# Optimization experiments

Hardware: AMD Instinct MI355X
Metric: run time of the kernel (lower is better)

The kernel has to match this reference:

```python
import jax, jax.numpy as jnp
import numpy as np
import math

H, W = 64, 64
WS = 8            # window_size
KS = 8            # kernel_size (depthwise conv stride=kernel)
D = 512           # d_model
CF = 128          # flow_dModel
IC = D + CF       # 640
HEAD = 8
GH, GW = H // WS, W // WS
G = GH * GW       # windows
EPS = 1e-5


def layernorm(x, g, b):
    m = jnp.mean(x, axis=-1, keepdims=True)
    v = jnp.mean((x - m) ** 2, axis=-1, keepdims=True)
    return (x - m) * jax.lax.rsqrt(v + EPS) * g + b


def depthwise_conv(x_nchw, w, b):
    # w: [C, 1, KS, KS], stride=KS, VALID, groups=C
    y = jax.lax.conv_general_dilated(
        x_nchw, w, window_strides=(KS, KS), padding='VALID',
        feature_group_count=x_nchw.shape[1],
        dimension_numbers=('NCHW', 'OIHW', 'NCHW'))
    return y + b[None, :, None, None]


def setup_inputs() -> dict:
    key = jax.random.key(0)
    ks = jax.random.split(key, 24)
    bt = 8
    s = 0.02
    inp = {
        'x': jax.random.normal(ks[0], (bt, H * W, D), jnp.float32),
        'f': jax.random.normal(ks[1], (bt, H * W, CF), jnp.float32),
        't': 2,
        'Wq': jax.random.normal(ks[2], (IC, D), jnp.float32) * s,
        'bq': jnp.zeros((D,), jnp.float32),
        'Wk': jax.random.normal(ks[3], (IC, D), jnp.float32) * s,
        'bk': jnp.zeros((D,), jnp.float32),
        'Wv': jax.random.normal(ks[4], (D, D), jnp.float32) * s,
        'bv': jnp.zeros((D,), jnp.float32),
        'Wo': jax.random.normal(ks[5], (D, D), jnp.float32) * s,
        'bo': jnp.zeros((D,), jnp.float32),
        'convK_w': jax.random.normal(ks[6], (IC, 1, KS, KS), jnp.float32) * s,
        'convK_b': jnp.zeros((IC,), jnp.float32),
        'convV_w': jax.random.normal(ks[7], (D, 1, KS, KS), jnp.float32) * s,
        'convV_b': jnp.zeros((D,), jnp.float32),
        'qn_g': jnp.ones((IC,), jnp.float32), 'qn_b': jnp.zeros((IC,), jnp.float32),
        'kn_g': jnp.ones((IC,), jnp.float32), 'kn_b': jnp.zeros((IC,), jnp.float32),
        'vn_g': jnp.ones((D,), jnp.float32), 'vn_b': jnp.zeros((D,), jnp.float32),
        'rw_W': jax.random.normal(ks[8], (IC, CF), jnp.float32) * s,
        'rw_b': jnp.zeros((CF,), jnp.float32),
    }
    return inp


def reference(x, f, t, Wq, bq, Wk, bk, Wv, bv, Wo, bo,
              convK_w, convK_b, convV_w, convV_b,
              qn_g, qn_b, kn_g, kn_b, vn_g, vn_b, rw_W, rw_b):
    bt, n, c = x.shape
    hd = c // HEAD
    x4 = x.reshape(bt, H, W, c)            # no padding: H, W multiples of WS
    f4 = f.reshape(bt, H, W, CF)

    xf = jnp.concatenate([x4, f4], axis=-1)                 # [bt,H,W,IC]
    flow_w = jax.nn.sigmoid(xf @ rw_W + rw_b)               # [bt,H,W,CF]
    f4 = f4 * flow_w
    qk = jnp.concatenate([x4, f4], axis=-1)                 # [bt,H,W,IC]

    def windows(a):
        cc = a.shape[-1]
        a = a.reshape(bt, GH, WS, GW, WS, cc).transpose(0, 1, 3, 2, 4, 5)
        return a.reshape(bt, G, WS * WS, cc)

    q = windows(qk)                                          # [bt,G,ws2,IC]

    k_glob = depthwise_conv(qk.transpose(0, 3, 1, 2), convK_w, convK_b)
    k_glob = k_glob.transpose(0, 2, 3, 1).reshape(bt, -1, IC)  # [bt,M,IC]
    M = k_glob.shape[1]
    k_glob = jnp.broadcast_to(k_glob[:, None], (bt, G, M, IC))
    k = jnp.concatenate([q, k_glob], axis=2)                 # [bt,G,ws2+M,IC]

    q = layernorm(q, qn_g, qn_b)
    k = layernorm(k, kn_g, kn_b)

    v_glob = depthwise_conv(x4.transpose(0, 3, 1, 2), convV_w, convV_b)
    v_glob = v_glob.transpose(0, 2, 3, 1).reshape(bt, -1, c)
    v_glob = jnp.broadcast_to(v_glob[:, None], (bt, G, M, c))
    xw = windows(x4)
    v = jnp.concatenate([xw, v_glob], axis=2)                # [bt,G,ws2+M,c]
    v = layernorm(v, vn_g, vn_b)

    query = q @ Wq + bq                                      # [bt,G,ws2,c]
    key = k @ Wk + bk
    value = v @ Wv + bv

    Lk = key.shape[2]
    query = query.reshape(bt, G, WS * WS, HEAD, hd).transpose(0, 1, 3, 2, 4)
    key = key.reshape(bt, G, Lk, HEAD, hd).transpose(0, 1, 3, 2, 4)
    value = value.reshape(bt, G, Lk, HEAD, hd).transpose(0, 1, 3, 2, 4)

    scores = jnp.einsum('bghqd,bghkd->bghqk', query, key) / math.sqrt(hd)
    attn = jax.nn.softmax(scores, axis=-1)
    out = jnp.einsum('bghqk,bghkd->bghqd', attn, value)      # [bt,G,H,ws2,hd]

    out = out.transpose(0, 1, 3, 2, 4).reshape(bt, GH, GW, WS, WS, c)
    out = out.transpose(0, 1, 3, 2, 4, 5).reshape(bt, H, W, c).reshape(bt, n, c)
    return out @ Wo + bo
```

## Files before the change

### kernel.cpp

```cpp
#include <hip/hip_runtime.h>
#include <hip/hip_bf16.h>

typedef __hip_bfloat16 bf16;
typedef __attribute__((ext_vector_type(8))) short bf16x8;
typedef __attribute__((ext_vector_type(8))) unsigned short ushort8;
typedef __attribute__((ext_vector_type(4))) float f32x4;

#define BT 8
#define HH 64
#define WW 64
#define NSP (HH*WW)
#define DD 512
#define CF 128
#define IC 640
#define NG 64
#define NM 64
#define EPS 1e-5f

static __device__ __forceinline__ float b2f(bf16 v) { return __bfloat162float(v); }
static __device__ __forceinline__ bf16 f2b(float v) { return __float2bfloat16(v); }
static __device__ __forceinline__ float u2f(unsigned short u) {
    return __uint_as_float((unsigned)u << 16);
}
static __device__ __forceinline__ unsigned short f2u(float v) {
    bf16 b = __float2bfloat16(v);
    return __builtin_bit_cast(unsigned short, b);
}

__global__ void detect_dtype(const void* __restrict__ x, int* __restrict__ flag) {
    __shared__ int cnt;
    if (threadIdx.x == 0) cnt = 0;
    __syncthreads();
    const unsigned* w = (const unsigned*)x;
    int local = 0;
    for (int i = threadIdx.x; i < 4096; i += 256) {
        float v = __uint_as_float(w[i]);
        float a = fabsf(v);
        if (a > 1e-5f && a < 1e4f) local++;
    }
    atomicAdd(&cnt, local);
    __syncthreads();
    if (threadIdx.x == 0) *flag = (cnt > 2048) ? 1 : 0;
}

#define NW 20
struct WTab {
    const void* src[NW];
    int pre[NW + 1];
};

__global__ void convert_weights(WTab t, const int* __restrict__ flag,
                                bf16* __restrict__ dst, int total) {
    int fp32 = *flag;
    for (int idx = blockIdx.x * blockDim.x + threadIdx.x; idx < total;
         idx += gridDim.x * blockDim.x) {
        int seg = 0;
        #pragma unroll
        for (int i = 0; i < NW; ++i) if (idx >= t.pre[i + 1]) seg = i + 1;
        int local = idx - t.pre[seg];
        bf16 v;
        if (fp32) v = f2b(((const float*)t.src[seg])[local]);
        else      v = ((const bf16*)t.src[seg])[local];
        dst[idx] = v;
    }
}

struct TT {
    int srcoff[5], dstoff[5], R[5], C[5], tpre[6];
};
__global__ void transpose_weights(const bf16* __restrict__ wc, bf16* __restrict__ wt, TT t) {
    __shared__ unsigned short tile[32][33];
    int tb = blockIdx.x;
    int seg = 0;
    while (tb >= t.tpre[seg + 1]) seg++;
    int lt = tb - t.tpre[seg];
    int R = t.R[seg], C = t.C[seg];
    int tpr = C / 32;
    int r0 = (lt / tpr) * 32, c0 = (lt % tpr) * 32;
    const unsigned short* src = (const unsigned short*)(wc + t.srcoff[seg]);
    unsigned short* dst = (unsigned short*)(wt + t.dstoff[seg]);
    int tx = threadIdx.x & 31, ty = threadIdx.x >> 5;
    #pragma unroll
    for (int i = 0; i < 4; ++i)
        tile[ty + i * 8][tx] = src[(long long)(r0 + ty + i * 8) * C + c0 + tx];
    __syncthreads();
    #pragma unroll
    for (int i = 0; i < 4; ++i)
        dst[(long long)(c0 + ty + i * 8) * R + r0 + tx] = tile[tx][ty + i * 8];
}

__global__ void fold_ln_weights(bf16* __restrict__ WT, const bf16* __restrict__ g,
                                const bf16* __restrict__ b, const bf16* __restrict__ bias,
                                float* __restrict__ colsum, float* __restrict__ bias2,
                                int K) {
    int n = blockIdx.x;
    bf16* wrow = WT + (long long)n * K;
    float s1 = 0.f, s2 = 0.f;
    for (int k = threadIdx.x; k < K; k += 256) {
        float w = b2f(wrow[k]);
        float gk = b2f(g[k]);
        wrow[k] = f2b(w * gk);
        s1 += w * gk;
        s2 += w * b2f(b[k]);
    }
    __shared__ float r1[256], r2[256];
    r1[threadIdx.x] = s1; r2[threadIdx.x] = s2;
    __syncthreads();
    for (int off = 128; off > 0; off >>= 1) {
        if (threadIdx.x < off) {
            r1[threadIdx.x] += r1[threadIdx.x + off];
            r2[threadIdx.x] += r2[threadIdx.x + off];
        }
        __syncthreads();
    }
    if (threadIdx.x == 0) {
        colsum[n] = r1[0];
        bias2[n]  = b2f(bias[n]) + r2[0];
    }
}

__global__ void assemble_qk_v(const void* __restrict__ xv, const void* __restrict__ fv,
                              const int* __restrict__ flag, bf16* __restrict__ qk,
                              int rows, long long xoff, long long foff) {
    int fp32 = *flag;
    long long total = (long long)rows * 80;
    for (long long i = (long long)blockIdx.x * blockDim.x + threadIdx.x; i < total;
         i += (long long)gridDim.x * blockDim.x) {
        int row = (int)(i / 80);
        int g = (int)(i % 80);
        ushort8 o;
        if (g < 64) {
            long long s = xoff + (long long)row * DD + g * 8;
            if (fp32) {
                const float* xp = (const float*)xv + s;
                #pragma unroll
                for (int e = 0; e < 8; ++e) o[e] = f2u(xp[e]);
            } else {
                o = *(const ushort8*)((const unsigned short*)xv + s);
            }
        } else {
            long long s = foff + (long long)row * CF + (g - 64) * 8;
            if (fp32) {
                const float* fp = (const float*)fv + s;
                #pragma unroll
                for (int e = 0; e < 8; ++e) o[e] = f2u(fp[e]);
            } else {
                o = *(const ushort8*)((const unsigned short*)fv + s);
            }
        }
        *(ushort8*)((unsigned short*)qk + (long long)row * IC + g * 8) = o;
    }
}

__global__ void reweight_v(bf16* __restrict__ qk, const bf16* __restrict__ fw, int rows) {
    long long total = (long long)rows * 16;
    long long i = (long long)blockIdx.x * blockDim.x + threadIdx.x;
    if (i >= total) return;
    int row = (int)(i / 16);
    int g = (int)(i % 16);
    unsigned short* qp = (unsigned short*)qk + (long long)row * IC + DD + g * 8;
    const unsigned short* wp = (const unsigned short*)fw + (long long)row * CF + g * 8;
    ushort8 qv = *(ushort8*)qp;
    ushort8 wv = *(const ushort8*)wp;
    #pragma unroll
    for (int e = 0; e < 8; ++e) qv[e] = f2u(u2f(qv[e]) * u2f(wv[e]));
    *(ushort8*)qp = qv;
}

__global__ void dwconv_kernel(const bf16* __restrict__ src, int ldr, int C, int ldout,
                              const bf16* __restrict__ w, const bf16* __restrict__ bias,
                              bf16* __restrict__ dst) {
    int bm = blockIdx.x;
    int b = bm >> 6;
    int m = bm & 63;
    int my = m >> 3, mx = m & 7;
    const bf16* sb = src + (long long)b * NSP * ldr;
    for (int c = threadIdx.x; c < C; c += blockDim.x) {
        float acc = b2f(bias[c]);
        #pragma unroll
        for (int ky = 0; ky < 8; ++ky) {
            #pragma unroll
            for (int kx = 0; kx < 8; ++kx) {
                int pos = (my * 8 + ky) * WW + mx * 8 + kx;
                acc += b2f(sb[(long long)pos * ldr + c]) * b2f(w[c * 64 + ky * 8 + kx]);
            }
        }
        dst[(long long)bm * ldout + c] = f2b(acc);
    }
}

__global__ void stats_fused(const bf16* __restrict__ qk, float* __restrict__ stats_full,
                            float* __restrict__ stats_x, int rows) {
    int gt = blockIdx.x * blockDim.x + threadIdx.x;
    int wid = gt >> 6;
    int lane = gt & 63;
    if (wid >= rows) return;
    const unsigned short* p = (const unsigned short*)qk + (long long)wid * IC;
    ushort8 v = *(const ushort8*)(p + lane * 8);
    float s1 = 0.f, ss1 = 0.f, s2 = 0.f, ss2 = 0.f;
    #pragma unroll
    for (int e = 0; e < 8; ++e) { float f = u2f(v[e]); s1 += f; ss1 += f * f; }
    if (lane < 16) {
        ushort8 v2 = *(const ushort8*)(p + DD + lane * 8);
        #pragma unroll
        for (int e = 0; e < 8; ++e) { float f = u2f(v2[e]); s2 += f; ss2 += f * f; }
    }
    #pragma unroll
    for (int off = 32; off > 0; off >>= 1) {
        s1  += __shfl_down(s1,  off, 64);
        ss1 += __shfl_down(ss1, off, 64);
        s2  += __shfl_down(s2,  off, 64);
        ss2 += __shfl_down(ss2, off, 64);
    }
    if (lane == 0) {
        float m1 = s1 / 512.f;
        float var1 = ss1 / 512.f - m1 * m1;
        stats_x[wid * 2]     = m1;
        stats_x[wid * 2 + 1] = rsqrtf(var1 + EPS);
        float st = s1 + s2, sst = ss1 + ss2;
        float m2 = st / 640.f;
        float var2 = sst / 640.f - m2 * m2;
        stats_full[wid * 2]     = m2;
        stats_full[wid * 2 + 1] = rsqrtf(var2 + EPS);
    }
}

__global__ void stats_kernel(const bf16* __restrict__ X, int lda, float* __restrict__ stats,
                             int rows, int K) {
    int gt = blockIdx.x * blockDim.x + threadIdx.x;
    int wid = gt >> 6;
    int lane = gt & 63;
    if (wid >= rows) return;
    const bf16* p = X + (long long)wid * lda;
    float s = 0.f, ss = 0.f;
    for (int k = lane; k < K; k += 64) {
        float v = b2f(p[k]);
        s += v; ss += v * v;
    }
    #pragma unroll
    for (int off = 32; off > 0; off >>= 1) {
        s  += __shfl_down(s,  off, 64);
        ss += __shfl_down(ss, off, 64);
    }
    if (lane == 0) {
        float m = s / K;
        float var = ss / K - m * m;
        stats[wid * 2]     = m;
        stats[wid * 2 + 1] = rsqrtf(var + EPS);
    }
}

__global__ __launch_bounds__(256)
void gemm_mfma(const bf16* __restrict__ A, int lda,
               const float* __restrict__ stats,
               const float* __restrict__ colsum,
               const float* __restrict__ bias2,
               const bf16* __restrict__ Bmat,
               const bf16* __restrict__ bias,
               bf16* __restrict__ C,
               void* __restrict__ Cout, const int* __restrict__ outflag, long long outoff,
               const bf16* __restrict__ A2, const float* __restrict__ stats2,
               bf16* __restrict__ C2, int M2,
               int M, int N, int K, int mode) {
    __shared__ unsigned short As[128 * 32];
    __shared__ unsigned short Bs[128 * 32];
    int tid = threadIdx.x;

    int nwgx = gridDim.x;
    int nwg = nwgx * gridDim.y;
    int orig = blockIdx.y * nwgx + blockIdx.x;
    int qq = nwg >> 3, rr = nwg & 7;
    int xcd = orig & 7, idx = orig >> 3;
    int wg = (xcd < rr ? xcd * (qq + 1) : rr * (qq + 1) + (xcd - rr) * qq) + idx;
    int gy = wg / nwgx;
    int gx = wg % nwgx;
    int bn = gx * 128;

    int nby_main = M >> 7;
    const bf16* Ap;
    const float* stp;
    int rowbase, mlim, glob;
    if (gy < nby_main) {
        Ap = A; stp = stats; rowbase = gy * 128; mlim = M; glob = 0;
    } else {
        Ap = A2; stp = stats2; rowbase = (gy - nby_main) * 128; mlim = M2; glob = 1;
    }

    int wave = tid >> 6, lane = tid & 63;
    int qm = (wave >> 1) * 64;
    int qn = (wave & 1) * 64;
    int lm = lane & 15;
    int kq = (lane >> 4) * 8;
    int sr = lane >> 2;
    int sc = (lane & 3) * 8;

    f32x4 acc[4][4];
    #pragma unroll
    for (int i = 0; i < 4; ++i)
        #pragma unroll
        for (int j = 0; j < 4; ++j)
            acc[i][j] = (f32x4){0.f, 0.f, 0.f, 0.f};

    const unsigned short* Au = (const unsigned short*)Ap;
    const unsigned short* Bu = (const unsigned short*)Bmat;

    for (int k0 = 0; k0 < K; k0 += 32) {
        #pragma unroll
        for (int i = 0; i < 2; ++i) {
            int seg = wave * 2 + i;
            const unsigned short* gp =
                Au + (long long)(rowbase + seg * 16 + sr) * lda + k0 + sc;
            __builtin_amdgcn_global_load_lds(
                (const __attribute__((address_space(1))) void*)gp,
                (__attribute__((address_space(3))) void*)&As[seg * 512], 16, 0, 0);
        }
        #pragma unroll
        for (int i = 0; i < 2; ++i) {
            int seg = wave * 2 + i;
            const unsigned short* gp =
                Bu + (long long)(bn + seg * 16 + sr) * K + k0 + sc;
            __builtin_amdgcn_global_load_lds(
                (const __attribute__((address_space(1))) void*)gp,
                (__attribute__((address_space(3))) void*)&Bs[seg * 512], 16, 0, 0);
        }
        __syncthreads();
        bf16x8 af[4], bfr[4];
        #pragma unroll
        for (int i = 0; i < 4; ++i)
            af[i] = *(const bf16x8*)&As[(qm + i * 16 + lm) * 32 + kq];
        #pragma unroll
        for (int j = 0; j < 4; ++j)
            bfr[j] = *(const bf16x8*)&Bs[(qn + j * 16 + lm) * 32 + kq];
        #pragma unroll
        for (int i = 0; i < 4; ++i)
            #pragma unroll
            for (int j = 0; j < 4; ++j)
                acc[i][j] = __builtin_amdgcn_mfma_f32_16x16x32_bf16(
                    af[i], bfr[j], acc[i][j], 0, 0, 0);
        __syncthreads();
    }

    int rq = (lane >> 4) * 4;
    float cs[4], bb[4];
    #pragma unroll
    for (int j = 0; j < 4; ++j) {
        int col = bn + qn + j * 16 + lm;
        if (mode == 2) { cs[j] = colsum[col]; bb[j] = bias2[col]; }
        else bb[j] = bias ? b2f(bias[col]) : 0.f;
    }
    int ofp = (!glob && outflag) ? *outflag : 0;
    #pragma unroll
    for (int i = 0; i < 4; ++i) {
        #pragma unroll
        for (int r = 0; r < 4; ++r) {
            int row = rowbase + qm + i * 16 + rq + r;
            float mean = 0.f, rstd = 0.f;
            if (mode == 2) { mean = stp[row * 2]; rstd = stp[row * 2 + 1]; }
            if (row >= mlim) continue;
            #pragma unroll
            for (int j = 0; j < 4; ++j) {
                int col = bn + qn + j * 16 + lm;
                float v = acc[i][j][r];
                if (mode == 2) v = rstd * (v - mean * cs[j]) + bb[j];
                else {
                    v += bb[j];
                    if (mode == 1) v = 1.f / (1.f + __expf(-v));
                }
                long long ci = (long long)row * N + col;
                if (glob) {
                    C2[ci] = f2b(v);
                } else if (outflag) {
                    if (ofp) ((float*)Cout)[outoff + ci] = v;
                    else     ((bf16*)Cout)[outoff + ci] = f2b(v);
                } else {
                    C[ci] = f2b(v);
                }
            }
        }
    }
}

#define QS_STRIDE 72
#define PS_STRIDE 136
__global__ __launch_bounds__(256)
void attn_kernel(const bf16* __restrict__ query,
                 const bf16* __restrict__ key_win, const bf16* __restrict__ key_glob,
                 const bf16* __restrict__ val_win, const bf16* __restrict__ val_glob,
                 bf16* __restrict__ attout) {
    int h = blockIdx.x & 7;
    int g = (blockIdx.x >> 3) & 63;
    int b = blockIdx.x >> 9;
    int gy = g >> 3, gx = g & 7;

    __shared__ unsigned short smem[64 * PS_STRIDE + 64 * PS_STRIDE];
    unsigned short* Qs = smem;
    unsigned short* Ks = smem + 64 * QS_STRIDE;
    unsigned short* Ps = smem;
    unsigned short* Vs = smem + 64 * PS_STRIDE;

    int tid = threadIdx.x;
    const unsigned short* Q  = (const unsigned short*)query;
    const unsigned short* KW = (const unsigned short*)key_win;
    const unsigned short* KG = (const unsigned short*)key_glob;
    const unsigned short* VW = (const unsigned short*)val_win;
    const unsigned short* VG = (const unsigned short*)val_glob;

    #pragma unroll
    for (int it = 0; it < 2; ++it) {
        int i = tid + it * 256;
        int t = i >> 3, dg = (i & 7) * 8;
        int ty = t >> 3, tx = t & 7;
        long long row = (long long)b * NSP + (gy * 8 + ty) * WW + gx * 8 + tx;
        *(ushort8*)&Qs[t * QS_STRIDE + dg] = *(const ushort8*)&Q[row * DD + h * 64 + dg];
    }
    #pragma unroll
    for (int it = 0; it < 4; ++it) {
        int i = tid + it * 256;
        int t = i >> 3, dg = (i & 7) * 8;
        long long srow;
        const unsigned short* kp;
        if (t < 64) {
            int ty = t >> 3, tx = t & 7;
            srow = (long long)b * NSP + (gy * 8 + ty) * WW + gx * 8 + tx;
            kp = KW;
        } else {
            srow = (long long)b * NM + (t - 64);
            kp = KG;
        }
        *(ushort8*)&Ks[t * QS_STRIDE + dg] = *(const ushort8*)&kp[srow * DD + h * 64 + dg];
    }
    __syncthreads();

    int wave = tid >> 6, lane = tid & 63;
    int m0 = wave * 16;
    int lm = lane & 15;
    int quad = lane >> 4;

    f32x4 sacc[8];
    #pragma unroll
    for (int j = 0; j < 8; ++j) sacc[j] = (f32x4){0.f, 0.f, 0.f, 0.f};
    #pragma unroll
    for (int ks = 0; ks < 2; ++ks) {
        int kq = quad * 8 + ks * 32;
        bf16x8 af = *(const bf16x8*)&Qs[(m0 + lm) * QS_STRIDE + kq];
        #pragma unroll
        for (int j = 0; j < 8; ++j) {
            bf16x8 bfr = *(const bf16x8*)&Ks[(j * 16 + lm) * QS_STRIDE + kq];
            sacc[j] = __builtin_amdgcn_mfma_f32_16x16x32_bf16(af, bfr, sacc[j], 0, 0, 0);
        }
    }
    float pinv[4];
    #pragma unroll
    for (int r = 0; r < 4; ++r) {
        float mx = -1e30f;
        #pragma unroll
        for (int j = 0; j < 8; ++j) {
            sacc[j][r] *= 0.125f;
            mx = fmaxf(mx, sacc[j][r]);
        }
        mx = fmaxf(mx, __shfl_xor(mx, 1, 64));
        mx = fmaxf(mx, __shfl_xor(mx, 2, 64));
        mx = fmaxf(mx, __shfl_xor(mx, 4, 64));
        mx = fmaxf(mx, __shfl_xor(mx, 8, 64));
        float l = 0.f;
        #pragma unroll
        for (int j = 0; j < 8; ++j) {
            float p = __expf(sacc[j][r] - mx);
            sacc[j][r] = p;
            l += p;
        }
        l += __shfl_xor(l, 1, 64);
        l += __shfl_xor(l, 2, 64);
        l += __shfl_xor(l, 4, 64);
        l += __shfl_xor(l, 8, 64);
        pinv[r] = 1.f / l;
    }
    __syncthreads();

    #pragma unroll
    for (int r = 0; r < 4; ++r) {
        int qrow = m0 + quad * 4 + r;
        #pragma unroll
        for (int j = 0; j < 8; ++j)
            Ps[qrow * PS_STRIDE + j * 16 + lm] = f2u(sacc[j][r] * pinv[r]);
    }
    #pragma unroll
    for (int it = 0; it < 4; ++it) {
        int i = tid + it * 256;
        int t = i & 127, dg = (i >> 7) * 8;
        long long srow;
        const unsigned short* vp;
        if (t < 64) {
            int ty = t >> 3, tx = t & 7;
            srow = (long long)b * NSP + (gy * 8 + ty) * WW + gx * 8 + tx;
            vp = VW;
        } else {
            srow = (long long)b * NM + (t - 64);
            vp = VG;
        }
        ushort8 v = *(const ushort8*)&vp[srow * DD + h * 64 + dg];
        #pragma unroll
        for (int e = 0; e < 8; ++e) Vs[(dg + e) * PS_STRIDE + t] = v[e];
    }
    __syncthreads();

    f32x4 oacc[4];
    #pragma unroll
    for (int j = 0; j < 4; ++j) oacc[j] = (f32x4){0.f, 0.f, 0.f, 0.f};
    #pragma unroll
    for (int ks = 0; ks < 4; ++ks) {
        int kq = quad * 8 + ks * 32;
        bf16x8 af = *(const bf16x8*)&Ps[(m0 + lm) * PS_STRIDE + kq];
        #pragma unroll
        for (int j = 0; j < 4; ++j) {
            bf16x8 bfr = *(const bf16x8*)&Vs[(j * 16 + lm) * PS_STRIDE + kq];
            oacc[j] = __builtin_amdgcn_mfma_f32_16x16x32_bf16(af, bfr, oacc[j], 0, 0, 0);
        }
    }
    #pragma unroll
    for (int r = 0; r < 4; ++r) {
        int qrow = m0 + quad * 4 + r;
        int ty = qrow >> 3, tx = qrow & 7;
        long long orow = (long long)b * NSP + (gy * 8 + ty) * WW + gx * 8 + tx;
        unsigned short* op = (unsigned short*)attout + orow * DD + h * 64;
        #pragma unroll
        for (int j = 0; j < 4; ++j)
            op[j * 16 + lm] = f2u(oacc[j][r]);
    }
}

static inline size_t alg(size_t b) { return (b + 255) & ~(size_t)255; }

extern "C" void kernel_launch(void* const* d_in, const int* in_sizes, int n_in,
                              void* d_out, int out_size, void* d_ws, size_t ws_size,
                              hipStream_t stream) {
    int s = (n_in > 2 && in_sizes[2] == 1) ? 0 : -1;

    const void* xv = d_in[0];
    const void* fv = d_in[1];
    const void* wsrc[NW];
    for (int i = 0; i < NW; ++i) wsrc[i] = d_in[3 + s + i];
    (void)out_size;

    const int wcnt[NW] = {327680, 512, 327680, 512, 262144, 512, 262144, 512,
                          40960, 640, 32768, 512, 640, 640, 640, 640, 512, 512,
                          81920, 128};
    WTab tab;
    int pre = 0;
    for (int i = 0; i < NW; ++i) {
        tab.src[i] = wsrc[i];
        tab.pre[i] = pre;
        pre += wcnt[i];
    }
    tab.pre[NW] = pre;
    const int wtotal = pre;

    char* ws = (char*)d_ws;
    size_t head = 0;
    int* flag = (int*)(ws + head); head += 256;
    bf16* wc = (bf16*)(ws + head); head += alg((size_t)wtotal * 2);
    const int wtcnt[5] = {327680, 327680, 262144, 262144, 81920};
    int wtoff[5], wtpre = 0;
    for (int i = 0; i < 5; ++i) { wtoff[i] = wtpre; wtpre += wtcnt[i]; }
    bf16* wt = (bf16*)(ws + head); head += alg((size_t)wtpre * 2);
    float* foldv = (float*)(ws + head); head += alg(6 * 512 * sizeof(float));
    float* cs_q = foldv;        float* b2_q = foldv + 512;
    float* cs_k = foldv + 1024; float* b2_k = foldv + 1536;
    float* cs_v = foldv + 2048; float* b2_v = foldv + 2560;

    const bf16* bq     = wc + tab.pre[1];
    const bf16* bk     = wc + tab.pre[3];
    const bf16* bv     = wc + tab.pre[5];
    const bf16* bo     = wc + tab.pre[7];
    const bf16* convKw = wc + tab.pre[8];
    const bf16* convKb = wc + tab.pre[9];
    const bf16* convVw = wc + tab.pre[10];
    const bf16* convVb = wc + tab.pre[11];
    const bf16* qn_g   = wc + tab.pre[12];
    const bf16* qn_b   = wc + tab.pre[13];
    const bf16* kn_g   = wc + tab.pre[14];
    const bf16* kn_b   = wc + tab.pre[15];
    const bf16* vn_g   = wc + tab.pre[16];
    const bf16* vn_b   = wc + tab.pre[17];
    const bf16* rw_b   = wc + tab.pre[19];
    bf16* WqT = wt + wtoff[0];
    bf16* WkT = wt + wtoff[1];
    bf16* WvT = wt + wtoff[2];
    bf16* WoT = wt + wtoff[3];
    bf16* rwT = wt + wtoff[4];

    size_t avail = ws_size > head ? ws_size - head : 0;
    auto need = [&](int bc) -> size_t {
        size_t rows = (size_t)bc * NSP;
        size_t gm = (size_t)bc * NM, gmp = gm + 64;
        return alg(rows * IC * 2) + 3 * alg(rows * DD * 2)
             + 2 * alg(gmp * IC * 2) + 2 * alg(gm * DD * 2)
             + 2 * alg(rows * 8) + 2 * alg(gmp * 8);
    };
    int nb = BT;
    while (nb > 1 && need(nb) > avail) nb--;

    detect_dtype<<<1, 256, 0, stream>>>(xv, flag);
    convert_weights<<<(wtotal + 255) / 256, 256, 0, stream>>>(tab, flag, wc, wtotal);
    {
        TT tt;
        const int srcsel[5] = {0, 2, 4, 6, 18};
        const int Rr[5] = {IC, IC, DD, DD, IC};
        const int Cc[5] = {DD, DD, DD, DD, CF};
        int tp = 0;
        for (int i = 0; i < 5; ++i) {
            tt.srcoff[i] = tab.pre[srcsel[i]];
            tt.dstoff[i] = wtoff[i];
            tt.R[i] = Rr[i];
            tt.C[i] = Cc[i];
            tt.tpre[i] = tp;
            tp += (Rr[i] / 32) * (Cc[i] / 32);
        }
        tt.tpre[5] = tp;
        transpose_weights<<<tp, 256, 0, stream>>>(wc, wt, tt);
    }
    fold_ln_weights<<<DD, 256, 0, stream>>>(WqT, qn_g, qn_b, bq, cs_q, b2_q, IC);
    fold_ln_weights<<<DD, 256, 0, stream>>>(WkT, kn_g, kn_b, bk, cs_k, b2_k, IC);
    fold_ln_weights<<<DD, 256, 0, stream>>>(WvT, vn_g, vn_b, bv, cs_v, b2_v, DD);

    for (int b0 = 0; b0 < BT; b0 += nb) {
        int bc = BT - b0 < nb ? BT - b0 : nb;
        int rows = bc * NSP;
        int gm = bc * NM;
        int gmp = gm + 64;
        int gyg = (gm + 127) / 128;

        size_t off = head;
        auto alloc = [&](size_t bytes) -> void* {
            void* p = ws + off; off += alg(bytes); return p;
        };
        bf16* qk        = (bf16*)alloc((size_t)rows * IC * 2);
        bf16* query     = (bf16*)alloc((size_t)rows * DD * 2);
        bf16* key_win   = (bf16*)alloc((size_t)rows * DD * 2);
        bf16* val_win   = (bf16*)alloc((size_t)rows * DD * 2);
        bf16* kg        = (bf16*)alloc((size_t)gmp * IC * 2);
        bf16* vg        = (bf16*)alloc((size_t)gmp * IC * 2);
        bf16* key_glob  = (bf16*)alloc((size_t)gm * DD * 2);
        bf16* val_glob  = (bf16*)alloc((size_t)gm * DD * 2);
        float* stats_qk = (float*)alloc((size_t)rows * 8);
        float* stats_x  = (float*)alloc((size_t)rows * 8);
        float* stats_kg = (float*)alloc((size_t)gmp * 8);
        float* stats_vg = (float*)alloc((size_t)gmp * 8);
        bf16* fw        = query;
        bf16* attout    = qk;

        {
            long long total = (long long)rows * 80;
            int blocks = (int)((total + 255) / 256);
            assemble_qk_v<<<blocks, 256, 0, stream>>>(
                xv, fv, flag, qk, rows,
                (long long)b0 * NSP * DD, (long long)b0 * NSP * CF);
        }
        gemm_mfma<<<dim3(CF / 128, rows / 128), 256, 0, stream>>>(
            qk, IC, nullptr, nullptr, nullptr, rwT, rw_b, fw,
            nullptr, nullptr, 0, nullptr, nullptr, nullptr, 0,
            rows, CF, IC, 1);
        {
            long long total = (long long)rows * 16;
            reweight_v<<<(int)((total + 255) / 256), 256, 0, stream>>>(qk, fw, rows);
        }
        dwconv_kernel<<<bc * NM, 256, 0, stream>>>(qk, IC, IC, IC, convKw, convKb, kg);
        dwconv_kernel<<<bc * NM, 256, 0, stream>>>(qk, IC, DD, IC, convVw, convVb, vg);
        stats_fused<<<rows / 4, 256, 0, stream>>>(qk, stats_qk, stats_x, rows);
        stats_kernel<<<(gm * 64 + 255) / 256, 256, 0, stream>>>(kg, IC, stats_kg, gm, IC);
        stats_kernel<<<(gm * 64 + 255) / 256, 256, 0, stream>>>(vg, IC, stats_vg, gm, DD);
        gemm_mfma<<<dim3(DD / 128, rows / 128), 256, 0, stream>>>(
            qk, IC, stats_qk, cs_q, b2_q, WqT, nullptr, query,
            nullptr, nullptr, 0, nullptr, nullptr, nullptr, 0,
            rows, DD, IC, 2);
        gemm_mfma<<<dim3(DD / 128, rows / 128 + gyg), 256, 0, stream>>>(
            qk, IC, stats_qk, cs_k, b2_k, WkT, nullptr, key_win,
            nullptr, nullptr, 0, kg, stats_kg, key_glob, gm,
            rows, DD, IC, 2);
        gemm_mfma<<<dim3(DD / 128, rows / 128 + gyg), 256, 0, stream>>>(
            qk, IC, stats_x, cs_v, b2_v, WvT, nullptr, val_win,
            nullptr, nullptr, 0, vg, stats_vg, val_glob, gm,
            rows, DD, DD, 2);
        attn_kernel<<<bc * NG * 8, 256, 0, stream>>>(query, key_win, key_glob,
                                                     val_win, val_glob, attout);
        gemm_mfma<<<dim3(DD / 128, rows / 128), 256, 0, stream>>>(
            attout, DD, nullptr, nullptr, nullptr, WoT, bo, nullptr,
            d_out, flag, (long long)b0 * NSP * DD,
            nullptr, nullptr, nullptr, 0,
            rows, DD, DD, 0);
    }
}
```

Before: 542.1 us.

## Fuse Q/K/V projections into one GEMM and fold reweight into sigmoid GEMM epilogue

Concatenates the transposed, LN-folded Wq, Wk and Wv into one [1536 x 640] weight matrix, with the V part zero-padded from 512 to 640 in K. This lets a single GEMM launch produce an interleaved qkv buffer that the attention kernel reads at stride 1536. The global key/value rows go through the same launch, with blocks dispatched by column range, and the separate reweight kernel is removed by applying the sigmoid-weighted multiply in place in a new mode-3 GEMM epilogue. The aim is fewer launches and better A-tile reuse across the three projections. In exchange, V does extra zero-padded K work, Q columns launch idle blocks on the global-row grid, and the epilogue does scalar read-modify-write stores.

```diff
diff --git a/kernel.cpp b/kernel.cpp
--- a/kernel.cpp
+++ b/kernel.cpp
@@ -15,6 +15,7 @@
 #define IC 640
 #define NG 64
 #define NM 64
+#define TRI 1536
 #define EPS 1e-5f
 
 static __device__ __forceinline__ float b2f(bf16 v) { return __bfloat162float(v); }
@@ -66,7 +67,7 @@
 }
 
 struct TT {
-    int srcoff[5], dstoff[5], R[5], C[5], tpre[6];
+    int srcoff[5], dstoff[5], R[5], C[5], dstride[5], tpre[6];
 };
 __global__ void transpose_weights(const bf16* __restrict__ wc, bf16* __restrict__ wt, TT t) {
     __shared__ unsigned short tile[32][33];
@@ -74,9 +75,10 @@
     int seg = 0;
     while (tb >= t.tpre[seg + 1]) seg++;
     int lt = tb - t.tpre[seg];
-    int R = t.R[seg], C = t.C[seg];
+    int C = t.C[seg];
     int tpr = C / 32;
     int r0 = (lt / tpr) * 32, c0 = (lt % tpr) * 32;
+    int ds = t.dstride[seg];
     const unsigned short* src = (const unsigned short*)(wc + t.srcoff[seg]);
     unsigned short* dst = (unsigned short*)(wt + t.dstoff[seg]);
     int tx = threadIdx.x & 31, ty = threadIdx.x >> 5;
@@ -86,15 +88,16 @@
     __syncthreads();
     #pragma unroll
     for (int i = 0; i < 4; ++i)
-        dst[(long long)(c0 + ty + i * 8) * R + r0 + tx] = tile[tx][ty + i * 8];
-}
-
-__global__ void fold_ln_weights(bf16* __restrict__ WT, const bf16* __restrict__ g,
+        dst[(long long)(c0 + ty + i * 8) * ds + r0 + tx] = tile[tx][ty + i * 8];
+}
+
+__global__ void fold_ln_weights(bf16* __restrict__ WT, int stride,
+                                const bf16* __restrict__ g,
                                 const bf16* __restrict__ b, const bf16* __restrict__ bias,
                                 float* __restrict__ colsum, float* __restrict__ bias2,
-                                int K) {
+                                int K, int Kpad) {
     int n = blockIdx.x;
-    bf16* wrow = WT + (long long)n * K;
+    bf16* wrow = WT + (long long)n * stride;
     float s1 = 0.f, s2 = 0.f;
     for (int k = threadIdx.x; k < K; k += 256) {
         float w = b2f(wrow[k]);
@@ -103,6 +106,7 @@
         s1 += w * gk;
         s2 += w * b2f(b[k]);
     }
+    for (int k = K + threadIdx.x; k < Kpad; k += 256) wrow[k] = f2b(0.f);
     __shared__ float r1[256], r2[256];
     r1[threadIdx.x] = s1; r2[threadIdx.x] = s2;
     __syncthreads();
@@ -152,22 +156,8 @@
     }
 }
 
-__global__ void reweight_v(bf16* __restrict__ qk, const bf16* __restrict__ fw, int rows) {
-    long long total = (long long)rows * 16;
-    long long i = (long long)blockIdx.x * blockDim.x + threadIdx.x;
-    if (i >= total) return;
-    int row = (int)(i / 16);
-    int g = (int)(i % 16);
-    unsigned short* qp = (unsigned short*)qk + (long long)row * IC + DD + g * 8;
-    const unsigned short* wp = (const unsigned short*)fw + (long long)row * CF + g * 8;
-    ushort8 qv = *(ushort8*)qp;
-    ushort8 wv = *(const ushort8*)wp;
-    #pragma unroll
-    for (int e = 0; e < 8; ++e) qv[e] = f2u(u2f(qv[e]) * u2f(wv[e]));
-    *(ushort8*)qp = qv;
-}
-
 __global__ void dwconv_kernel(const bf16* __restrict__ src, int ldr, int C, int ldout,
+                              int ldpad,
                               const bf16* __restrict__ w, const bf16* __restrict__ bias,
                               bf16* __restrict__ dst) {
     int bm = blockIdx.x;
@@ -187,6 +177,8 @@
         }
         dst[(long long)bm * ldout + c] = f2b(acc);
     }
+    for (int c = C + threadIdx.x; c < ldpad; c += blockDim.x)
+        dst[(long long)bm * ldout + c] = f2b(0.f);
 }
 
 __global__ void stats_fused(const bf16* __restrict__ qk, float* __restrict__ stats_full,
@@ -252,15 +244,17 @@
 
 __global__ __launch_bounds__(256)
 void gemm_mfma(const bf16* __restrict__ A, int lda,
-               const float* __restrict__ stats,
-               const float* __restrict__ colsum,
-               const float* __restrict__ bias2,
+               const float* __restrict__ statsQK, const float* __restrict__ statsX,
+               int nQK,
+               const float* __restrict__ colsum, const float* __restrict__ bias2,
                const bf16* __restrict__ Bmat,
                const bf16* __restrict__ bias,
                bf16* __restrict__ C,
                void* __restrict__ Cout, const int* __restrict__ outflag, long long outoff,
-               const bf16* __restrict__ A2, const float* __restrict__ stats2,
-               bf16* __restrict__ C2, int M2,
+               const bf16* __restrict__ A2k, const float* __restrict__ stats2k,
+               bf16* __restrict__ C2k,
+               const bf16* __restrict__ A2v, const float* __restrict__ stats2v,
+               bf16* __restrict__ C2v, int M2,
                int M, int N, int K, int mode) {
     __shared__ unsigned short As[128 * 32];
     __shared__ unsigned short Bs[128 * 32];
@@ -278,12 +272,20 @@
 
     int nby_main = M >> 7;
     const bf16* Ap;
-    const float* stp;
-    int rowbase, mlim, glob;
+    const float* stp = nullptr;
+    bf16* C2 = nullptr;
+    int rowbase, mlim, glob, colOff = 0;
     if (gy < nby_main) {
-        Ap = A; stp = stats; rowbase = gy * 128; mlim = M; glob = 0;
+        Ap = A; rowbase = gy * 128; mlim = M; glob = 0;
+        if (mode == 2) stp = (bn >= nQK) ? statsX : statsQK;
     } else {
-        Ap = A2; stp = stats2; rowbase = (gy - nby_main) * 128; mlim = M2; glob = 1;
+        if (bn < 512) return;
+        int isV = bn >= 1024;
+        Ap = isV ? A2v : A2k;
+        stp = isV ? stats2v : stats2k;
+        C2 = isV ? C2v : C2k;
+        colOff = isV ? 1024 : 512;
+        rowbase = (gy - nby_main) * 128; mlim = M2; glob = 1;
     }
 
     int wave = tid >> 6, lane = tid & 63;
@@ -354,9 +356,9 @@
         #pragma unroll
         for (int r = 0; r < 4; ++r) {
             int row = rowbase + qm + i * 16 + rq + r;
+            if (row >= mlim) continue;
             float mean = 0.f, rstd = 0.f;
             if (mode == 2) { mean = stp[row * 2]; rstd = stp[row * 2 + 1]; }
-            if (row >= mlim) continue;
             #pragma unroll
             for (int j = 0; j < 4; ++j) {
                 int col = bn + qn + j * 16 + lm;
@@ -364,16 +366,22 @@
                 if (mode == 2) v = rstd * (v - mean * cs[j]) + bb[j];
                 else {
                     v += bb[j];
-                    if (mode == 1) v = 1.f / (1.f + __expf(-v));
+                    if (mode == 1 || mode == 3) v = 1.f / (1.f + __expf(-v));
                 }
-                long long ci = (long long)row * N + col;
+                if (mode == 3) {
+                    unsigned short* qp =
+                        (unsigned short*)C + (long long)row * IC + DD + col;
+                    *qp = f2u(u2f(*qp) * v);
+                    continue;
+                }
                 if (glob) {
-                    C2[ci] = f2b(v);
+                    C2[(long long)row * 512 + (col - colOff)] = f2b(v);
                 } else if (outflag) {
+                    long long ci = (long long)row * N + col;
                     if (ofp) ((float*)Cout)[outoff + ci] = v;
                     else     ((bf16*)Cout)[outoff + ci] = f2b(v);
                 } else {
-                    C[ci] = f2b(v);
+                    C[(long long)row * N + col] = f2b(v);
                 }
             }
         }
@@ -383,9 +391,8 @@
 #define QS_STRIDE 72
 #define PS_STRIDE 136
 __global__ __launch_bounds__(256)
-void attn_kernel(const bf16* __restrict__ query,
-                 const bf16* __restrict__ key_win, const bf16* __restrict__ key_glob,
-                 const bf16* __restrict__ val_win, const bf16* __restrict__ val_glob,
+void attn_kernel(const bf16* __restrict__ qkv,
+                 const bf16* __restrict__ key_glob, const bf16* __restrict__ val_glob,
                  bf16* __restrict__ attout) {
     int h = blockIdx.x & 7;
     int g = (blockIdx.x >> 3) & 63;
@@ -399,10 +406,8 @@
     unsigned short* Vs = smem + 64 * PS_STRIDE;
 
     int tid = threadIdx.x;
-    const unsigned short* Q  = (const unsigned short*)query;
-    const unsigned short* KW = (const unsigned short*)key_win;
+    const unsigned short* QKV = (const unsigned short*)qkv;
     const unsigned short* KG = (const unsigned short*)key_glob;
-    const unsigned short* VW = (const unsigned short*)val_win;
     const unsigned short* VG = (const unsigned short*)val_glob;
 
     #pragma unroll
@@ -411,23 +416,23 @@
         int t = i >> 3, dg = (i & 7) * 8;
         int ty = t >> 3, tx = t & 7;
         long long row = (long long)b * NSP + (gy * 8 + ty) * WW + gx * 8 + tx;
-        *(ushort8*)&Qs[t * QS_STRIDE + dg] = *(const ushort8*)&Q[row * DD + h * 64 + dg];
+        *(ushort8*)&Qs[t * QS_STRIDE + dg] =
+            *(const ushort8*)&QKV[row * TRI + h * 64 + dg];
     }
     #pragma unroll
     for (int it = 0; it < 4; ++it) {
         int i = tid + it * 256;
         int t = i >> 3, dg = (i & 7) * 8;
-        long long srow;
-        const unsigned short* kp;
+        ushort8 kv;
         if (t < 64) {
             int ty = t >> 3, tx = t & 7;
-            srow = (long long)b * NSP + (gy * 8 + ty) * WW + gx * 8 + tx;
-            kp = KW;
+            long long row = (long long)b * NSP + (gy * 8 + ty) * WW + gx * 8 + tx;
+            kv = *(const ushort8*)&QKV[row * TRI + 512 + h * 64 + dg];
         } else {
-            srow = (long long)b * NM + (t - 64);
-            kp = KG;
-        }
-        *(ushort8*)&Ks[t * QS_STRIDE + dg] = *(const ushort8*)&kp[srow * DD + h * 64 + dg];
+            long long srow = (long long)b * NM + (t - 64);
+            kv = *(const ushort8*)&KG[srow * DD + h * 64 + dg];
+        }
+        *(ushort8*)&Ks[t * QS_STRIDE + dg] = kv;
     }
     __syncthreads();
 
@@ -488,17 +493,15 @@
     for (int it = 0; it < 4; ++it) {
         int i = tid + it * 256;
         int t = i & 127, dg = (i >> 7) * 8;
-        long long srow;
-        const unsigned short* vp;
+        ushort8 v;
         if (t < 64) {
             int ty = t >> 3, tx = t & 7;
-            srow = (long long)b * NSP + (gy * 8 + ty) * WW + gx * 8 + tx;
-            vp = VW;
+            long long row = (long long)b * NSP + (gy * 8 + ty) * WW + gx * 8 + tx;
+            v = *(const ushort8*)&QKV[row * TRI + 1024 + h * 64 + dg];
         } else {
-            srow = (long long)b * NM + (t - 64);
-            vp = VG;
-        }
-        ushort8 v = *(const ushort8*)&vp[srow * DD + h * 64 + dg];
+            long long srow = (long long)b * NM + (t - 64);
+            v = *(const ushort8*)&VG[srow * DD + h * 64 + dg];
+        }
         #pragma unroll
         for (int e = 0; e < 8; ++e) Vs[(dg + e) * PS_STRIDE + t] = v[e];
     }
@@ -559,14 +562,14 @@
     size_t head = 0;
     int* flag = (int*)(ws + head); head += 256;
     bf16* wc = (bf16*)(ws + head); head += alg((size_t)wtotal * 2);
-    const int wtcnt[5] = {327680, 327680, 262144, 262144, 81920};
-    int wtoff[5], wtpre = 0;
-    for (int i = 0; i < 5; ++i) { wtoff[i] = wtpre; wtpre += wtcnt[i]; }
+    const int off_qkvW = 0;
+    const int off_WoT  = TRI * IC;
+    const int off_rwT  = off_WoT + DD * DD;
+    const int wtpre    = off_rwT + CF * IC;
     bf16* wt = (bf16*)(ws + head); head += alg((size_t)wtpre * 2);
-    float* foldv = (float*)(ws + head); head += alg(6 * 512 * sizeof(float));
-    float* cs_q = foldv;        float* b2_q = foldv + 512;
-    float* cs_k = foldv + 1024; float* b2_k = foldv + 1536;
-    float* cs_v = foldv + 2048; float* b2_v = foldv + 2560;
+    float* foldv = (float*)(ws + head); head += alg(2 * TRI * sizeof(float));
+    float* cs_qkv = foldv;
+    float* b2_qkv = foldv + TRI;
 
     const bf16* bq     = wc + tab.pre[1];
     const bf16* bk     = wc + tab.pre[3];
@@ -583,17 +586,15 @@
     const bf16* vn_g   = wc + tab.pre[16];
     const bf16* vn_b   = wc + tab.pre[17];
     const bf16* rw_b   = wc + tab.pre[19];
-    bf16* WqT = wt + wtoff[0];
-    bf16* WkT = wt + wtoff[1];
-    bf16* WvT = wt + wtoff[2];
-    bf16* WoT = wt + wtoff[3];
-    bf16* rwT = wt + wtoff[4];
+    bf16* qkvW = wt + off_qkvW;
+    bf16* WoT  = wt + off_WoT;
+    bf16* rwT  = wt + off_rwT;
 
     size_t avail = ws_size > head ? ws_size - head : 0;
     auto need = [&](int bc) -> size_t {
         size_t rows = (size_t)bc * NSP;
         size_t gm = (size_t)bc * NM, gmp = gm + 64;
-        return alg(rows * IC * 2) + 3 * alg(rows * DD * 2)
+        return alg(rows * IC * 2) + alg(rows * TRI * 2)
              + 2 * alg(gmp * IC * 2) + 2 * alg(gm * DD * 2)
              + 2 * alg(rows * 8) + 2 * alg(gmp * 8);
     };
@@ -604,24 +605,30 @@
     convert_weights<<<(wtotal + 255) / 256, 256, 0, stream>>>(tab, flag, wc, wtotal);
     {
         TT tt;
-        const int srcsel[5] = {0, 2, 4, 6, 18};
-        const int Rr[5] = {IC, IC, DD, DD, IC};
-        const int Cc[5] = {DD, DD, DD, DD, CF};
+        const int srcsel[5]  = {0, 2, 4, 6, 18};
+        const int Rr[5]      = {IC, IC, DD, DD, IC};
+        const int Cc[5]      = {DD, DD, DD, DD, CF};
+        const int dof[5]     = {0, DD * IC, 2 * DD * IC, off_WoT, off_rwT};
+        const int dstr[5]    = {IC, IC, IC, DD, IC};
         int tp = 0;
         for (int i = 0; i < 5; ++i) {
             tt.srcoff[i] = tab.pre[srcsel[i]];
-            tt.dstoff[i] = wtoff[i];
+            tt.dstoff[i] = dof[i];
             tt.R[i] = Rr[i];
             tt.C[i] = Cc[i];
+            tt.dstride[i] = dstr[i];
             tt.tpre[i] = tp;
             tp += (Rr[i] / 32) * (Cc[i] / 32);
         }
         tt.tpre[5] = tp;
         transpose_weights<<<tp, 256, 0, stream>>>(wc, wt, tt);
     }
-    fold_ln_weights<<<DD, 256, 0, stream>>>(WqT, qn_g, qn_b, bq, cs_q, b2_q, IC);
-    fold_ln_weights<<<DD, 256, 0, stream>>>(WkT, kn_g, kn_b, bk, cs_k, b2_k, IC);
-    fold_ln_weights<<<DD, 256, 0, stream>>>(WvT, vn_g, vn_b, bv, cs_v, b2_v, DD);
+    fold_ln_weights<<<DD, 256, 0, stream>>>(qkvW,              IC, qn_g, qn_b, bq,
+                                            cs_qkv,       b2_qkv,       IC, IC);
+    fold_ln_weights<<<DD, 256, 0, stream>>>(qkvW + DD * IC,    IC, kn_g, kn_b, bk,
+                                            cs_qkv + 512, b2_qkv + 512, IC, IC);
+    fold_ln_weights<<<DD, 256, 0, stream>>>(qkvW + 2 * DD * IC, IC, vn_g, vn_b, bv,
+                                            cs_qkv + 1024, b2_qkv + 1024, DD, IC);
 
     for (int b0 = 0; b0 < BT; b0 += nb) {
         int bc = BT - b0 < nb ? BT - b0 : nb;
@@ -635,9 +642,7 @@
             void* p = ws + off; off += alg(bytes); return p;
         };
         bf16* qk        = (bf16*)alloc((size_t)rows * IC * 2);
-        bf16* query     = (bf16*)alloc((size_t)rows * DD * 2);
-        bf16* key_win   = (bf16*)alloc((size_t)rows * DD * 2);
-        bf16* val_win   = (bf16*)alloc((size_t)rows * DD * 2);
+        bf16* qkv       = (bf16*)alloc((size_t)rows * TRI * 2);
         bf16* kg        = (bf16*)alloc((size_t)gmp * IC * 2);
         bf16* vg        = (bf16*)alloc((size_t)gmp * IC * 2);
         bf16* key_glob  = (bf16*)alloc((size_t)gm * DD * 2);
@@ -646,7 +651,6 @@
         float* stats_x  = (float*)alloc((size_t)rows * 8);
         float* stats_kg = (float*)alloc((size_t)gmp * 8);
         float* stats_vg = (float*)alloc((size_t)gmp * 8);
-        bf16* fw        = query;
         bf16* attout    = qk;
 
         {
@@ -657,36 +661,25 @@
                 (long long)b0 * NSP * DD, (long long)b0 * NSP * CF);
         }
         gemm_mfma<<<dim3(CF / 128, rows / 128), 256, 0, stream>>>(
-            qk, IC, nullptr, nullptr, nullptr, rwT, rw_b, fw,
-            nullptr, nullptr, 0, nullptr, nullptr, nullptr, 0,
-            rows, CF, IC, 1);
-        {
-            long long total = (long long)rows * 16;
-            reweight_v<<<(int)((total + 255) / 256), 256, 0, stream>>>(qk, fw, rows);
-        }
-        dwconv_kernel<<<bc * NM, 256, 0, stream>>>(qk, IC, IC, IC, convKw, convKb, kg);
-        dwconv_kernel<<<bc * NM, 256, 0, stream>>>(qk, IC, DD, IC, convVw, convVb, vg);
+            qk, IC, nullptr, nullptr, 0, nullptr, nullptr, rwT, rw_b, qk,
+            nullptr, nullptr, 0,
+            nullptr, nullptr, nullptr, nullptr, nullptr, nullptr, 0,
+            rows, CF, IC, 3);
+        dwconv_kernel<<<bc * NM, 256, 0, stream>>>(qk, IC, IC, IC, IC, convKw, convKb, kg);
+        dwconv_kernel<<<bc * NM, 256, 0, stream>>>(qk, IC, DD, IC, IC, convVw, convVb, vg);
         stats_fused<<<rows / 4, 256, 0, stream>>>(qk, stats_qk, stats_x, rows);
         stats_kernel<<<(gm * 64 + 255) / 256, 256, 0, stream>>>(kg, IC, stats_kg, gm, IC);
         stats_kernel<<<(gm * 64 + 255) / 256, 256, 0, stream>>>(vg, IC, stats_vg, gm, DD);
+        gemm_mfma<<<dim3(TRI / 128, rows / 128 + gyg), 256, 0, stream>>>(
+            qk, IC, stats_qk, stats_x, 1024, cs_qkv, b2_qkv, qkvW, nullptr, qkv,
+            nullptr, nullptr, 0,
+            kg, stats_kg, key_glob, vg, stats_vg, val_glob, gm,
+            rows, TRI, IC, 2);
+        attn_kernel<<<bc * NG * 8, 256, 0, stream>>>(qkv, key_glob, val_glob, attout);
         gemm_mfma<<<dim3(DD / 128, rows / 128), 256, 0, stream>>>(
-            qk, IC, stats_qk, cs_q, b2_q, WqT, nullptr, query,
-            nullptr, nullptr, 0, nullptr, nullptr, nullptr, 0,
-            rows, DD, IC, 2);
-        gemm_mfma<<<dim3(DD / 128, rows / 128 + gyg), 256, 0, stream>>>(
-            qk, IC, stats_qk, cs_k, b2_k, WkT, nullptr, key_win,
-            nullptr, nullptr, 0, kg, stats_kg, key_glob, gm,
-            rows, DD, IC, 2);
-        gemm_mfma<<<dim3(DD / 128, rows / 128 + gyg), 256, 0, stream>>>(
-            qk, IC, stats_x, cs_v, b2_v, WvT, nullptr, val_win,
-            nullptr, nullptr, 0, vg, stats_vg, val_glob, gm,
-            rows, DD, DD, 2);
-        attn_kernel<<<bc * NG * 8, 256, 0, stream>>>(query, key_win, key_glob,
-                                                     val_win, val_glob, attout);
-        gemm_mfma<<<dim3(DD / 128, rows / 128), 256, 0, stream>>>(
-            attout, DD, nullptr, nullptr, nullptr, WoT, bo, nullptr,
+            attout, DD, nullptr, nullptr, 0, nullptr, nullptr, WoT, bo, nullptr,
             d_out, flag, (long long)b0 * NSP * DD,
-            nullptr, nullptr, nullptr, 0,
+            nullptr, nullptr, nullptr, nullptr, nullptr, nullptr, 0,
             rows, DD, DD, 0);
     }
 }
```

Measured after the change: 514.3 us. -5.1%, faster.
